# Kernel tuning notes

Hardware: AMD Instinct MI355X
Metric: run time of the kernel (lower is better)

The kernel has to match this reference:

```python
import jax, jax.numpy as jnp
import numpy as np

B, T, D, H, L = 64, 512, 512, 512, 2


def setup_inputs() -> dict:
    key = jax.random.key(0)
    ks = jax.random.split(key, 9)
    std = 1.0 / np.sqrt(H)
    u = lambda k, shape: jax.random.uniform(k, shape, jnp.float32, -std, std)
    return {
        "x": jax.random.normal(ks[0], (B, T, D), jnp.float32),
        "Wx0": u(ks[1], (4 * H, D)), "bx0": u(ks[2], (4 * H,)),
        "Wh0": u(ks[3], (4 * H, H)), "bh0": u(ks[4], (4 * H,)),
        "Wx1": u(ks[5], (4 * H, H)), "bx1": u(ks[6], (4 * H,)),
        "Wh1": u(ks[7], (4 * H, H)), "bh1": u(ks[8], (4 * H,)),
    }


def _lstm_layer(x_seq, Wx, bx, Wh, bh):
    # x_seq: [T, B, D_in] -> hidden sequence [T, B, H]
    h0 = jnp.zeros((x_seq.shape[1], Wh.shape[1]), x_seq.dtype)
    c0 = jnp.zeros_like(h0)
    # precompute input projections for all steps (one big GEMM)
    xg = jnp.einsum('tbd,gd->tbg', x_seq, Wx) + bx + bh  # [T, B, 4H]

    def step(carry, xg_t):
        h, c = carry
        gates = xg_t + h @ Wh.T
        f, i, g, o = jnp.split(gates, 4, axis=1)
        f = jax.nn.sigmoid(f)
        i = jax.nn.sigmoid(i)
        g = jnp.tanh(g)
        o = jax.nn.sigmoid(o)
        c = f * c + i * g
        h = o * jnp.tanh(c)
        return (h, c), h

    (_, _), hs = jax.lax.scan(step, (h0, c0), xg)
    return hs


def reference(x, Wx0, bx0, Wh0, bh0, Wx1, bx1, Wh1, bh1):
    xs = jnp.transpose(x, (1, 0, 2))  # [T, B, D]
    h1 = _lstm_layer(xs, Wx0, bx0, Wh0, bh0)   # [T, B, H]
    h2 = _lstm_layer(h1, Wx1, bx1, Wh1, bh1)   # [T, B, H]
    return h2[-1]  # last hidden state of top layer: [B, H]
```

## Files before the change

kernel.cpp:

```cpp
#include <hip/hip_runtime.h>
#include <hip/hip_bf16.h>
#include <stdint.h>

#define T_STEPS 512
#define BATCH   64
#define HID     512
#define DIN     512
#define G4      2048
#define HBLK_T  32768
#define SENT8   0xFFFFFFFFFFFFFFFFull

typedef __attribute__((ext_vector_type(8))) short bf16x8;
typedef __attribute__((ext_vector_type(4))) float f32x4;
typedef __attribute__((ext_vector_type(4))) unsigned short us4;

static __device__ __forceinline__ unsigned short f2bf(float f) {
  union { float f; unsigned u; } v; v.f = f;
  unsigned r = v.u + 0x7FFFu + ((v.u >> 16) & 1u);
  return (unsigned short)(r >> 16);
}
static __device__ __forceinline__ float bf2f(unsigned short s) {
  union { unsigned u; float f; } v; v.u = ((unsigned)s) << 16;
  return v.f;
}
static __device__ __forceinline__ float sigf(float x) { return 1.f / (1.f + __expf(-x)); }
static __device__ __forceinline__ float tanh_fast(float x) {
  x = fminf(15.f, fmaxf(-15.f, x));
  float e = __expf(2.f * x);
  return (e - 1.f) / (e + 1.f);
}

__global__ void cvt_f32_bf16(const float* __restrict__ src, unsigned short* __restrict__ dst, long n) {
  long i = (long)blockIdx.x * blockDim.x + threadIdx.x;
  long st = (long)gridDim.x * blockDim.x;
  for (; i < n; i += st) dst[i] = f2bf(src[i]);
}

__global__ void bias_sum(const float* __restrict__ a, const float* __restrict__ b,
                         float* __restrict__ o, int n) {
  int i = blockIdx.x * blockDim.x + threadIdx.x;
  if (i < n) o[i] = a[i] + b[i];
}

__global__ __launch_bounds__(256) void proj_kernel(
    const float* __restrict__ x,
    const unsigned short* __restrict__ Wb,
    const float* __restrict__ bias,
    unsigned short* __restrict__ xg) {
  __shared__ unsigned short xt[64 * 512];
  const int t   = blockIdx.x;
  const int tid = threadIdx.x;

  for (int i = 0; i < 16; ++i) {
    const int c    = i * 256 + tid;
    const int b    = c >> 6;
    const int col8 = c & 63;
    const float* src = x + ((long)b * T_STEPS + t) * DIN + col8 * 8;
    f32x4 v0 = *(const f32x4*)(src);
    f32x4 v1 = *(const f32x4*)(src + 4);
    union { unsigned short s[8]; bf16x8 v; } u;
    #pragma unroll
    for (int e = 0; e < 4; ++e) { u.s[e] = f2bf(v0[e]); u.s[4 + e] = f2bf(v1[e]); }
    const int byteoff = b * 1024 + ((col8 * 16) ^ ((b & 7) << 4));
    *(bf16x8*)((char*)xt + byteoff) = u.v;
  }
  __syncthreads();

  const int wv   = tid >> 6;
  const int lane = tid & 63;
  const int n16  = lane & 15;
  const int q    = lane >> 4;
  const int kof  = q * 8;

  for (int gt = 0; gt < 32; ++gt) {
    const int g0 = wv * 512 + gt * 16;
    const unsigned short* ap = Wb + (long)(g0 + n16) * DIN + kof;
    f32x4 acc[4];
    #pragma unroll
    for (int nb = 0; nb < 4; ++nb) acc[nb] = (f32x4){0.f, 0.f, 0.f, 0.f};
    #pragma unroll
    for (int kk = 0; kk < 16; ++kk) {
      bf16x8 a = *(const bf16x8*)(ap + kk * 32);
      const int colb = (kof + kk * 32) * 2;
      #pragma unroll
      for (int nb = 0; nb < 4; ++nb) {
        const int row = nb * 16 + n16;
        bf16x8 bv = *(const bf16x8*)((const char*)xt + row * 1024 + (colb ^ ((row & 7) << 4)));
        acc[nb] = __builtin_amdgcn_mfma_f32_16x16x32_bf16(a, bv, acc[nb], 0, 0, 0);
      }
    }
    const int m0 = q * 4;
    #pragma unroll
    for (int r = 0; r < 4; ++r) {
      const int g = g0 + m0 + r;
      const float bv = bias[g];
      long base = ((long)t * G4 + g) * BATCH + n16;
      xg[base +  0] = f2bf(acc[0][r] + bv);
      xg[base + 16] = f2bf(acc[1][r] + bv);
      xg[base + 32] = f2bf(acc[2][r] + bv);
      xg[base + 48] = f2bf(acc[3][r] + bv);
    }
  }
}

__global__ __launch_bounds__(128) void fused_rec(
    const unsigned short* __restrict__ Wh0b,
    const unsigned short* __restrict__ xg0,
    const unsigned short* __restrict__ Wx1b,
    const unsigned short* __restrict__ Wh1b,
    const float* __restrict__ bs1,
    unsigned short* __restrict__ hseq1,
    unsigned short* __restrict__ hseq2,
    float* __restrict__ out,
    int T) {
  __shared__ unsigned short whl0[32 * 512];
  __shared__ unsigned short whl1[32 * 1024];
  __shared__ __align__(16) unsigned short hsc[2][128];

  const int bid  = blockIdx.x;
  const int gq   = bid & 3;
  const int j    = bid >> 2;
  const int wv   = threadIdx.x >> 6;
  const int lane = threadIdx.x & 63;
  const int hidbase = j * 8;
  const int n16  = lane & 15;
  const int q    = lane >> 4;
  const int kof  = q * 8;
  const int bloc = q * 4;
  const int rr0 = n16, rr1 = 16 + n16;
  const int grow0 = (rr0 >> 3) * HID + hidbase + (rr0 & 7);
  const int grow1 = (rr1 >> 3) * HID + hidbase + (rr1 & 7);
  const int rdbase = gq * 128 + n16 * 8;
  const int myblk  = (j * 4 + gq) * 128;

  if (wv == 0) {
    #pragma unroll 4
    for (int r = 0; r < 32; ++r) {
      const long grow = (long)(r >> 3) * HID + hidbase + (r & 7);
      bf16x8 v = *(const bf16x8*)(Wh0b + grow * HID + lane * 8);
      const int off = r * 1024 + ((lane * 16) ^ ((r & 7) << 4));
      *(bf16x8*)((char*)whl0 + off) = v;
    }
  } else {
    #pragma unroll 2
    for (int r = 0; r < 32; ++r) {
      const long grow = (long)(r >> 3) * HID + hidbase + (r & 7);
      bf16x8 va = *(const bf16x8*)(Wx1b + grow * HID + lane * 8);
      bf16x8 vb = *(const bf16x8*)(Wh1b + grow * HID + lane * 8);
      const int rb = r * 2048;
      *(bf16x8*)((char*)whl1 + rb + ((lane * 16) ^ ((r & 7) << 4))) = va;
      *(bf16x8*)((char*)whl1 + rb + ((1024 + lane * 16) ^ ((r & 7) << 4))) = vb;
    }
  }
  __syncthreads();

  if (wv == 0) {
    float c[4] = {0.f, 0.f, 0.f, 0.f};
    for (int t = 0; t < T; ++t) {
      us4 xv0 = *(const us4*)(xg0 + ((long)t * G4 + grow0) * BATCH + gq * 16 + bloc);
      us4 xv1 = *(const us4*)(xg0 + ((long)t * G4 + grow1) * BATCH + gq * 16 + bloc);

      f32x4 acc0 = {0.f,0.f,0.f,0.f}, acc1 = {0.f,0.f,0.f,0.f};
      if (t > 0) {
        const unsigned long long* hp = (const unsigned long long*)
            (hseq1 + (long)(t - 1) * HBLK_T + rdbase);
        unsigned long long lo[16], hi[16];
        int bad;
        do {
          bad = 0;
          #pragma unroll
          for (int kk = 0; kk < 16; ++kk) {
            const int boff = (kk * 4 + q) * 128;
            lo[kk] = __hip_atomic_load(hp + boff,     __ATOMIC_RELAXED, __HIP_MEMORY_SCOPE_AGENT);
            hi[kk] = __hip_atomic_load(hp + boff + 1, __ATOMIC_RELAXED, __HIP_MEMORY_SCOPE_AGENT);
          }
          #pragma unroll
          for (int kk = 0; kk < 16; ++kk)
            bad |= (lo[kk] == SENT8) | (hi[kk] == SENT8);
        } while (__any(bad));
        #pragma unroll
        for (int kk = 0; kk < 16; ++kk) {
          union { unsigned long long qq[2]; bf16x8 v; } u;
          u.qq[0] = lo[kk]; u.qq[1] = hi[kk];
          const int colb = (kof + kk * 32) * 2;
          bf16x8 b0 = *(const bf16x8*)((const char*)whl0 + rr0 * 1024 + (colb ^ ((rr0 & 7) << 4)));
          bf16x8 b1 = *(const bf16x8*)((const char*)whl0 + rr1 * 1024 + (colb ^ ((rr1 & 7) << 4)));
          acc0 = __builtin_amdgcn_mfma_f32_16x16x32_bf16(u.v, b0, acc0, 0, 0, 0);
          acc1 = __builtin_amdgcn_mfma_f32_16x16x32_bf16(u.v, b1, acc1, 0, 0, 0);
        }
      }
      #pragma unroll
      for (int r = 0; r < 4; ++r) { acc0[r] += bf2f(xv0[r]); acc1[r] += bf2f(xv1[r]); }

      f32x4 o0, o1;
      #pragma unroll
      for (int r = 0; r < 4; ++r) {
        o0[r] = __shfl_xor(acc0[r], 8, 64);
        o1[r] = __shfl_xor(acc1[r], 8, 64);
      }
      if (n16 < 8) {
        #pragma unroll
        for (int r = 0; r < 4; ++r) {
          const float fg = sigf(acc0[r]);
          const float ig = sigf(o0[r]);
          const float gg = tanh_fast(acc1[r]);
          const float og = sigf(o1[r]);
          const float cn = fg * c[r] + ig * gg;
          c[r] = cn;
          const float h = og * tanh_fast(cn);
          *(unsigned short*)((char*)hsc[0] + (bloc + r) * 16 + n16 * 2) = f2bf(h);
        }
      }
      asm volatile("s_waitcnt lgkmcnt(0)" ::: "memory");
      if (lane < 32) {
        unsigned long long v8 = *(const unsigned long long*)((const char*)hsc[0] + lane * 8);
        unsigned long long* dst = (unsigned long long*)
            (hseq1 + (long)t * HBLK_T + myblk) + lane;
        __hip_atomic_store(dst, v8, __ATOMIC_RELAXED, __HIP_MEMORY_SCOPE_AGENT);
      }
    }
  } else {
    float c[4] = {0.f, 0.f, 0.f, 0.f};
    const float b0v = bs1[grow0], b1v = bs1[grow1];
    for (int t = 0; t < T; ++t) {
      f32x4 acc0 = {0.f,0.f,0.f,0.f}, acc1 = {0.f,0.f,0.f,0.f};
      {
        const unsigned long long* hp = (const unsigned long long*)
            (hseq1 + (long)t * HBLK_T + rdbase);
        unsigned long long lo[16], hi[16];
        int bad;
        do {
          bad = 0;
          #pragma unroll
          for (int kk = 0; kk < 16; ++kk) {
            const int boff = (kk * 4 + q) * 128;
            lo[kk] = __hip_atomic_load(hp + boff,     __ATOMIC_RELAXED, __HIP_MEMORY_SCOPE_AGENT);
            hi[kk] = __hip_atomic_load(hp + boff + 1, __ATOMIC_RELAXED, __HIP_MEMORY_SCOPE_AGENT);
          }
          #pragma unroll
          for (int kk = 0; kk < 16; ++kk)
            bad |= (lo[kk] == SENT8) | (hi[kk] == SENT8);
        } while (__any(bad));
        #pragma unroll
        for (int kk = 0; kk < 16; ++kk) {
          union { unsigned long long qq[2]; bf16x8 v; } u;
          u.qq[0] = lo[kk]; u.qq[1] = hi[kk];
          const int colb = (kof + kk * 32) * 2;
          bf16x8 b0 = *(const bf16x8*)((const char*)whl1 + rr0 * 2048 + (colb ^ ((rr0 & 7) << 4)));
          bf16x8 b1 = *(const bf16x8*)((const char*)whl1 + rr1 * 2048 + (colb ^ ((rr1 & 7) << 4)));
          acc0 = __builtin_amdgcn_mfma_f32_16x16x32_bf16(u.v, b0, acc0, 0, 0, 0);
          acc1 = __builtin_amdgcn_mfma_f32_16x16x32_bf16(u.v, b1, acc1, 0, 0, 0);
        }
      }
      if (t > 0) {
        const unsigned long long* hp = (const unsigned long long*)
            (hseq2 + (long)(t - 1) * HBLK_T + rdbase);
        unsigned long long lo[16], hi[16];
        int bad;
        do {
          bad = 0;
          #pragma unroll
          for (int kk = 0; kk < 16; ++kk) {
            const int boff = (kk * 4 + q) * 128;
            lo[kk] = __hip_atomic_load(hp + boff,     __ATOMIC_RELAXED, __HIP_MEMORY_SCOPE_AGENT);
            hi[kk] = __hip_atomic_load(hp + boff + 1, __ATOMIC_RELAXED, __HIP_MEMORY_SCOPE_AGENT);
          }
          #pragma unroll
          for (int kk = 0; kk < 16; ++kk)
            bad |= (lo[kk] == SENT8) | (hi[kk] == SENT8);
        } while (__any(bad));
        #pragma unroll
        for (int kk = 0; kk < 16; ++kk) {
          union { unsigned long long qq[2]; bf16x8 v; } u;
          u.qq[0] = lo[kk]; u.qq[1] = hi[kk];
          const int colb = 1024 + (kof + kk * 32) * 2;
          bf16x8 b0 = *(const bf16x8*)((const char*)whl1 + rr0 * 2048 + (colb ^ ((rr0 & 7) << 4)));
          bf16x8 b1 = *(const bf16x8*)((const char*)whl1 + rr1 * 2048 + (colb ^ ((rr1 & 7) << 4)));
          acc0 = __builtin_amdgcn_mfma_f32_16x16x32_bf16(u.v, b0, acc0, 0, 0, 0);
          acc1 = __builtin_amdgcn_mfma_f32_16x16x32_bf16(u.v, b1, acc1, 0, 0, 0);
        }
      }
      #pragma unroll
      for (int r = 0; r < 4; ++r) { acc0[r] += b0v; acc1[r] += b1v; }

      f32x4 o0, o1;
      #pragma unroll
      for (int r = 0; r < 4; ++r) {
        o0[r] = __shfl_xor(acc0[r], 8, 64);
        o1[r] = __shfl_xor(acc1[r], 8, 64);
      }
      if (n16 < 8) {
        const int hid = hidbase + n16;
        #pragma unroll
        for (int r = 0; r < 4; ++r) {
          const float fg = sigf(acc0[r]);
          const float ig = sigf(o0[r]);
          const float gg = tanh_fast(acc1[r]);
          const float og = sigf(o1[r]);
          const float cn = fg * c[r] + ig * gg;
          c[r] = cn;
          const float h = og * tanh_fast(cn);
          *(unsigned short*)((char*)hsc[1] + (bloc + r) * 16 + n16 * 2) = f2bf(h);
          if (t == T - 1) out[(long)(gq * 16 + bloc + r) * HID + hid] = h;
        }
      }
      asm volatile("s_waitcnt lgkmcnt(0)" ::: "memory");
      if (lane < 32) {
        unsigned long long v8 = *(const unsigned long long*)((const char*)hsc[1] + lane * 8);
        unsigned long long* dst = (unsigned long long*)
            (hseq2 + (long)t * HBLK_T + myblk) + lane;
        __hip_atomic_store(dst, v8, __ATOMIC_RELAXED, __HIP_MEMORY_SCOPE_AGENT);
      }
    }
  }
}

extern "C" void kernel_launch(void* const* d_in, const int* in_sizes, int n_in,
                              void* d_out, int out_size, void* d_ws, size_t ws_size,
                              hipStream_t stream) {
  const float* x   = (const float*)d_in[0];
  const float* Wx0 = (const float*)d_in[1];
  const float* bx0 = (const float*)d_in[2];
  const float* Wh0 = (const float*)d_in[3];
  const float* bh0 = (const float*)d_in[4];
  const float* Wx1 = (const float*)d_in[5];
  const float* bx1 = (const float*)d_in[6];
  const float* Wh1 = (const float*)d_in[7];
  const float* bh1 = (const float*)d_in[8];

  char* ws = (char*)d_ws;
  size_t off = 0;
  auto alloc = [&](size_t bytes) -> char* {
    char* p = ws + off; off += (bytes + 255) & ~(size_t)255; return p;
  };
  unsigned short* xg    = (unsigned short*)alloc((size_t)T_STEPS * G4 * BATCH * 2);
  unsigned short* hseq1 = (unsigned short*)alloc((size_t)T_STEPS * HBLK_T * 2);
  unsigned short* hseq2 = (unsigned short*)alloc((size_t)T_STEPS * HBLK_T * 2);
  unsigned short* Wx0b  = (unsigned short*)alloc((size_t)G4 * DIN * 2);
  unsigned short* Wh0b  = (unsigned short*)alloc((size_t)G4 * HID * 2);
  unsigned short* Wx1b  = (unsigned short*)alloc((size_t)G4 * HID * 2);
  unsigned short* Wh1b  = (unsigned short*)alloc((size_t)G4 * HID * 2);
  float* bs0 = (float*)alloc((size_t)G4 * 4);
  float* bs1 = (float*)alloc((size_t)G4 * 4);

  hipMemsetAsync(hseq1, 0xFF, (size_t)T_STEPS * HBLK_T * 2, stream);
  hipMemsetAsync(hseq2, 0xFF, (size_t)T_STEPS * HBLK_T * 2, stream);

  cvt_f32_bf16<<<1024, 256, 0, stream>>>(Wx0, Wx0b, (long)G4 * DIN);
  cvt_f32_bf16<<<1024, 256, 0, stream>>>(Wh0, Wh0b, (long)G4 * HID);
  cvt_f32_bf16<<<1024, 256, 0, stream>>>(Wx1, Wx1b, (long)G4 * HID);
  cvt_f32_bf16<<<1024, 256, 0, stream>>>(Wh1, Wh1b, (long)G4 * HID);
  bias_sum<<<8, 256, 0, stream>>>(bx0, bh0, bs0, G4);
  bias_sum<<<8, 256, 0, stream>>>(bx1, bh1, bs1, G4);

  proj_kernel<<<T_STEPS, 256, 0, stream>>>(x, Wx0b, bs0, xg);
  fused_rec<<<256, 128, 0, stream>>>(Wh0b, xg, Wx1b, Wh1b, bs1,
                                     hseq1, hseq2, (float*)d_out, T_STEPS);
}
```

Before: 2.043 ms.

## Fuse layer-0 input projection into recurrent kernel via producer wave and LDS ring

The separate projection GEMM and the weight and bias conversion kernels are removed. A third wave in each recurrent block now computes the layer-0 input projection for its own gate rows step by step and hands the results to the layer-0 wave through a 16-slot shared-memory ring, synchronised with workgroup-scope flags. Weights are converted from fp32 inside the kernel, and the h-sequence loads are issued before waiting on the ring. This removes the large xg round trip through global memory and several launches, but adds an extra wave per block and intra-block spin waits.

New measurement: 2.278 ms. 11.5% more time.

```diff
diff --git a/kernel.cpp b/kernel.cpp
--- a/kernel.cpp
+++ b/kernel.cpp
@@ -8,11 +8,13 @@
 #define DIN     512
 #define G4      2048
 #define HBLK_T  32768
+#define RING    16
 #define SENT8   0xFFFFFFFFFFFFFFFFull
 
 typedef __attribute__((ext_vector_type(8))) short bf16x8;
 typedef __attribute__((ext_vector_type(4))) float f32x4;
 typedef __attribute__((ext_vector_type(4))) unsigned short us4;
+typedef unsigned long long ull;
 
 static __device__ __forceinline__ unsigned short f2bf(float f) {
   union { float f; unsigned u; } v; v.f = f;
@@ -30,92 +32,38 @@
   return (e - 1.f) / (e + 1.f);
 }
 
-__global__ void cvt_f32_bf16(const float* __restrict__ src, unsigned short* __restrict__ dst, long n) {
-  long i = (long)blockIdx.x * blockDim.x + threadIdx.x;
-  long st = (long)gridDim.x * blockDim.x;
-  for (; i < n; i += st) dst[i] = f2bf(src[i]);
-}
-
-__global__ void bias_sum(const float* __restrict__ a, const float* __restrict__ b,
-                         float* __restrict__ o, int n) {
-  int i = blockIdx.x * blockDim.x + threadIdx.x;
-  if (i < n) o[i] = a[i] + b[i];
-}
-
-__global__ __launch_bounds__(256) void proj_kernel(
-    const float* __restrict__ x,
-    const unsigned short* __restrict__ Wb,
-    const float* __restrict__ bias,
-    unsigned short* __restrict__ xg) {
-  __shared__ unsigned short xt[64 * 512];
-  const int t   = blockIdx.x;
-  const int tid = threadIdx.x;
-
-  for (int i = 0; i < 16; ++i) {
-    const int c    = i * 256 + tid;
-    const int b    = c >> 6;
-    const int col8 = c & 63;
-    const float* src = x + ((long)b * T_STEPS + t) * DIN + col8 * 8;
-    f32x4 v0 = *(const f32x4*)(src);
-    f32x4 v1 = *(const f32x4*)(src + 4);
-    union { unsigned short s[8]; bf16x8 v; } u;
-    #pragma unroll
-    for (int e = 0; e < 4; ++e) { u.s[e] = f2bf(v0[e]); u.s[4 + e] = f2bf(v1[e]); }
-    const int byteoff = b * 1024 + ((col8 * 16) ^ ((b & 7) << 4));
-    *(bf16x8*)((char*)xt + byteoff) = u.v;
-  }
-  __syncthreads();
-
-  const int wv   = tid >> 6;
-  const int lane = tid & 63;
-  const int n16  = lane & 15;
-  const int q    = lane >> 4;
-  const int kof  = q * 8;
-
-  for (int gt = 0; gt < 32; ++gt) {
-    const int g0 = wv * 512 + gt * 16;
-    const unsigned short* ap = Wb + (long)(g0 + n16) * DIN + kof;
-    f32x4 acc[4];
-    #pragma unroll
-    for (int nb = 0; nb < 4; ++nb) acc[nb] = (f32x4){0.f, 0.f, 0.f, 0.f};
-    #pragma unroll
-    for (int kk = 0; kk < 16; ++kk) {
-      bf16x8 a = *(const bf16x8*)(ap + kk * 32);
-      const int colb = (kof + kk * 32) * 2;
-      #pragma unroll
-      for (int nb = 0; nb < 4; ++nb) {
-        const int row = nb * 16 + n16;
-        bf16x8 bv = *(const bf16x8*)((const char*)xt + row * 1024 + (colb ^ ((row & 7) << 4)));
-        acc[nb] = __builtin_amdgcn_mfma_f32_16x16x32_bf16(a, bv, acc[nb], 0, 0, 0);
-      }
-    }
-    const int m0 = q * 4;
-    #pragma unroll
-    for (int r = 0; r < 4; ++r) {
-      const int g = g0 + m0 + r;
-      const float bv = bias[g];
-      long base = ((long)t * G4 + g) * BATCH + n16;
-      xg[base +  0] = f2bf(acc[0][r] + bv);
-      xg[base + 16] = f2bf(acc[1][r] + bv);
-      xg[base + 32] = f2bf(acc[2][r] + bv);
-      xg[base + 48] = f2bf(acc[3][r] + bv);
-    }
-  }
-}
-
-__global__ __launch_bounds__(128) void fused_rec(
-    const unsigned short* __restrict__ Wh0b,
-    const unsigned short* __restrict__ xg0,
-    const unsigned short* __restrict__ Wx1b,
-    const unsigned short* __restrict__ Wh1b,
-    const float* __restrict__ bs1,
+__global__ __launch_bounds__(256) void xb_cvt(const float* __restrict__ x,
+                                              unsigned short* __restrict__ xb) {
+  const long c  = (long)blockIdx.x * blockDim.x + threadIdx.x;
+  const int b   = (int)(c >> 15);
+  const int rem = (int)(c & 32767);
+  const int t   = rem >> 6;
+  const int k8  = rem & 63;
+  const float* src = x + ((long)b * T_STEPS + t) * DIN + k8 * 8;
+  f32x4 v0 = *(const f32x4*)src;
+  f32x4 v1 = *(const f32x4*)(src + 4);
+  union { unsigned short s[8]; bf16x8 v; } u;
+  #pragma unroll
+  for (int e = 0; e < 4; ++e) { u.s[e] = f2bf(v0[e]); u.s[4 + e] = f2bf(v1[e]); }
+  *(bf16x8*)(xb + ((long)t * BATCH + b) * DIN + k8 * 8) = u.v;
+}
+
+__global__ __launch_bounds__(192, 1) void fused_rec(
+    const float* __restrict__ Wh0, const float* __restrict__ Wx0,
+    const float* __restrict__ Wh1, const float* __restrict__ Wx1,
+    const float* __restrict__ bx0, const float* __restrict__ bh0,
+    const float* __restrict__ bx1, const float* __restrict__ bh1,
+    const unsigned short* __restrict__ xb,
     unsigned short* __restrict__ hseq1,
     unsigned short* __restrict__ hseq2,
     float* __restrict__ out,
     int T) {
+  __shared__ unsigned short wx0l[32 * 512];
   __shared__ unsigned short whl0[32 * 512];
   __shared__ unsigned short whl1[32 * 1024];
+  __shared__ __align__(16) unsigned short ring[RING][512];
   __shared__ __align__(16) unsigned short hsc[2][128];
+  __shared__ int p_done, l0_done;
 
   const int bid  = blockIdx.x;
   const int gq   = bid & 3;
@@ -133,55 +81,76 @@
   const int rdbase = gq * 128 + n16 * 8;
   const int myblk  = (j * 4 + gq) * 128;
 
+  if (threadIdx.x == 0) { p_done = 0; l0_done = 0; }
+
+  auto cv8 = [](const float* s) -> bf16x8 {
+    f32x4 a = *(const f32x4*)s, b = *(const f32x4*)(s + 4);
+    union { unsigned short u[8]; bf16x8 v; } w;
+    #pragma unroll
+    for (int e = 0; e < 4; ++e) { w.u[e] = f2bf(a[e]); w.u[4 + e] = f2bf(b[e]); }
+    return w.v;
+  };
   if (wv == 0) {
-    #pragma unroll 4
     for (int r = 0; r < 32; ++r) {
       const long grow = (long)(r >> 3) * HID + hidbase + (r & 7);
-      bf16x8 v = *(const bf16x8*)(Wh0b + grow * HID + lane * 8);
-      const int off = r * 1024 + ((lane * 16) ^ ((r & 7) << 4));
-      *(bf16x8*)((char*)whl0 + off) = v;
-    }
-  } else {
-    #pragma unroll 2
+      bf16x8 v = cv8(Wh0 + grow * HID + lane * 8);
+      *(bf16x8*)((char*)whl0 + r * 1024 + ((lane * 16) ^ ((r & 7) << 4))) = v;
+    }
+  } else if (wv == 1) {
     for (int r = 0; r < 32; ++r) {
       const long grow = (long)(r >> 3) * HID + hidbase + (r & 7);
-      bf16x8 va = *(const bf16x8*)(Wx1b + grow * HID + lane * 8);
-      bf16x8 vb = *(const bf16x8*)(Wh1b + grow * HID + lane * 8);
+      bf16x8 va = cv8(Wx1 + grow * HID + lane * 8);
+      bf16x8 vb = cv8(Wh1 + grow * HID + lane * 8);
       const int rb = r * 2048;
       *(bf16x8*)((char*)whl1 + rb + ((lane * 16) ^ ((r & 7) << 4))) = va;
       *(bf16x8*)((char*)whl1 + rb + ((1024 + lane * 16) ^ ((r & 7) << 4))) = vb;
     }
+  } else {
+    for (int r = 0; r < 32; ++r) {
+      const long grow = (long)(r >> 3) * HID + hidbase + (r & 7);
+      bf16x8 v = cv8(Wx0 + grow * HID + lane * 8);
+      *(bf16x8*)((char*)wx0l + r * 1024 + ((lane * 16) ^ ((r & 7) << 4))) = v;
+    }
   }
   __syncthreads();
 
   if (wv == 0) {
-    float c[4] = {0.f, 0.f, 0.f, 0.f};
+    float c4[4] = {0.f, 0.f, 0.f, 0.f};
     for (int t = 0; t < T; ++t) {
-      us4 xv0 = *(const us4*)(xg0 + ((long)t * G4 + grow0) * BATCH + gq * 16 + bloc);
-      us4 xv1 = *(const us4*)(xg0 + ((long)t * G4 + grow1) * BATCH + gq * 16 + bloc);
+      ull lo[16], hi[16];
+      const ull* hp = (const ull*)(hseq1 + (long)(t - 1) * HBLK_T + rdbase);
+      if (t > 0) {
+        #pragma unroll
+        for (int kk = 0; kk < 16; ++kk) {
+          const int boff = (kk * 4 + q) * 128;
+          lo[kk] = __hip_atomic_load(hp + boff,     __ATOMIC_RELAXED, __HIP_MEMORY_SCOPE_AGENT);
+          hi[kk] = __hip_atomic_load(hp + boff + 1, __ATOMIC_RELAXED, __HIP_MEMORY_SCOPE_AGENT);
+        }
+      }
+      while (__hip_atomic_load(&p_done, __ATOMIC_ACQUIRE, __HIP_MEMORY_SCOPE_WORKGROUP) < t + 1) {}
+      const int s = t & (RING - 1);
+      us4 xv0 = *(const us4*)&ring[s][n16 * 16 + q * 4];
+      us4 xv1 = *(const us4*)&ring[s][(16 + n16) * 16 + q * 4];
+      if (lane == 0)
+        __hip_atomic_store(&l0_done, t + 1, __ATOMIC_RELEASE, __HIP_MEMORY_SCOPE_WORKGROUP);
 
       f32x4 acc0 = {0.f,0.f,0.f,0.f}, acc1 = {0.f,0.f,0.f,0.f};
       if (t > 0) {
-        const unsigned long long* hp = (const unsigned long long*)
-            (hseq1 + (long)(t - 1) * HBLK_T + rdbase);
-        unsigned long long lo[16], hi[16];
-        int bad;
-        do {
-          bad = 0;
+        for (;;) {
+          int bad = 0;
+          #pragma unroll
+          for (int kk = 0; kk < 16; ++kk) bad |= (lo[kk] == SENT8) | (hi[kk] == SENT8);
+          if (!__any(bad)) break;
           #pragma unroll
           for (int kk = 0; kk < 16; ++kk) {
             const int boff = (kk * 4 + q) * 128;
             lo[kk] = __hip_atomic_load(hp + boff,     __ATOMIC_RELAXED, __HIP_MEMORY_SCOPE_AGENT);
             hi[kk] = __hip_atomic_load(hp + boff + 1, __ATOMIC_RELAXED, __HIP_MEMORY_SCOPE_AGENT);
           }
-          #pragma unroll
-          for (int kk = 0; kk < 16; ++kk)
-            bad |= (lo[kk] == SENT8) | (hi[kk] == SENT8);
-        } while (__any(bad));
-        #pragma unroll
-        for (int kk = 0; kk < 16; ++kk) {
-          union { unsigned long long qq[2]; bf16x8 v; } u;
-          u.qq[0] = lo[kk]; u.qq[1] = hi[kk];
+        }
+        #pragma unroll
+        for (int kk = 0; kk < 16; ++kk) {
+          union { ull qq[2]; bf16x8 v; } u; u.qq[0] = lo[kk]; u.qq[1] = hi[kk];
           const int colb = (kof + kk * 32) * 2;
           bf16x8 b0 = *(const bf16x8*)((const char*)whl0 + rr0 * 1024 + (colb ^ ((rr0 & 7) << 4)));
           bf16x8 b1 = *(const bf16x8*)((const char*)whl0 + rr1 * 1024 + (colb ^ ((rr1 & 7) << 4)));
@@ -205,74 +174,79 @@
           const float ig = sigf(o0[r]);
           const float gg = tanh_fast(acc1[r]);
           const float og = sigf(o1[r]);
-          const float cn = fg * c[r] + ig * gg;
-          c[r] = cn;
+          const float cn = fg * c4[r] + ig * gg;
+          c4[r] = cn;
           const float h = og * tanh_fast(cn);
           *(unsigned short*)((char*)hsc[0] + (bloc + r) * 16 + n16 * 2) = f2bf(h);
         }
       }
       asm volatile("s_waitcnt lgkmcnt(0)" ::: "memory");
       if (lane < 32) {
-        unsigned long long v8 = *(const unsigned long long*)((const char*)hsc[0] + lane * 8);
-        unsigned long long* dst = (unsigned long long*)
-            (hseq1 + (long)t * HBLK_T + myblk) + lane;
+        ull v8 = *(const ull*)((const char*)hsc[0] + lane * 8);
+        ull* dst = (ull*)(hseq1 + (long)t * HBLK_T + myblk) + lane;
         __hip_atomic_store(dst, v8, __ATOMIC_RELAXED, __HIP_MEMORY_SCOPE_AGENT);
       }
     }
-  } else {
-    float c[4] = {0.f, 0.f, 0.f, 0.f};
-    const float b0v = bs1[grow0], b1v = bs1[grow1];
+  } else if (wv == 1) {
+    float c4[4] = {0.f, 0.f, 0.f, 0.f};
+    const float b0v = bx1[grow0] + bh1[grow0];
+    const float b1v = bx1[grow1] + bh1[grow1];
     for (int t = 0; t < T; ++t) {
+      ull la[16], ha[16], lb[16], hb[16];
+      const ull* pa = (const ull*)(hseq1 + (long)t * HBLK_T + rdbase);
+      const ull* pb = (const ull*)(hseq2 + (long)(t - 1) * HBLK_T + rdbase);
+      #pragma unroll
+      for (int kk = 0; kk < 16; ++kk) {
+        const int boff = (kk * 4 + q) * 128;
+        la[kk] = __hip_atomic_load(pa + boff,     __ATOMIC_RELAXED, __HIP_MEMORY_SCOPE_AGENT);
+        ha[kk] = __hip_atomic_load(pa + boff + 1, __ATOMIC_RELAXED, __HIP_MEMORY_SCOPE_AGENT);
+      }
+      if (t > 0) {
+        #pragma unroll
+        for (int kk = 0; kk < 16; ++kk) {
+          const int boff = (kk * 4 + q) * 128;
+          lb[kk] = __hip_atomic_load(pb + boff,     __ATOMIC_RELAXED, __HIP_MEMORY_SCOPE_AGENT);
+          hb[kk] = __hip_atomic_load(pb + boff + 1, __ATOMIC_RELAXED, __HIP_MEMORY_SCOPE_AGENT);
+        }
+      }
+      for (;;) {
+        int bad = 0;
+        #pragma unroll
+        for (int kk = 0; kk < 16; ++kk) bad |= (la[kk] == SENT8) | (ha[kk] == SENT8);
+        if (!__any(bad)) break;
+        #pragma unroll
+        for (int kk = 0; kk < 16; ++kk) {
+          const int boff = (kk * 4 + q) * 128;
+          la[kk] = __hip_atomic_load(pa + boff,     __ATOMIC_RELAXED, __HIP_MEMORY_SCOPE_AGENT);
+          ha[kk] = __hip_atomic_load(pa + boff + 1, __ATOMIC_RELAXED, __HIP_MEMORY_SCOPE_AGENT);
+        }
+      }
       f32x4 acc0 = {0.f,0.f,0.f,0.f}, acc1 = {0.f,0.f,0.f,0.f};
-      {
-        const unsigned long long* hp = (const unsigned long long*)
-            (hseq1 + (long)t * HBLK_T + rdbase);
-        unsigned long long lo[16], hi[16];
-        int bad;
-        do {
-          bad = 0;
+      #pragma unroll
+      for (int kk = 0; kk < 16; ++kk) {
+        union { ull qq[2]; bf16x8 v; } u; u.qq[0] = la[kk]; u.qq[1] = ha[kk];
+        const int colb = (kof + kk * 32) * 2;
+        bf16x8 b0 = *(const bf16x8*)((const char*)whl1 + rr0 * 2048 + (colb ^ ((rr0 & 7) << 4)));
+        bf16x8 b1 = *(const bf16x8*)((const char*)whl1 + rr1 * 2048 + (colb ^ ((rr1 & 7) << 4)));
+        acc0 = __builtin_amdgcn_mfma_f32_16x16x32_bf16(u.v, b0, acc0, 0, 0, 0);
+        acc1 = __builtin_amdgcn_mfma_f32_16x16x32_bf16(u.v, b1, acc1, 0, 0, 0);
+      }
+      if (t > 0) {
+        for (;;) {
+          int bad = 0;
+          #pragma unroll
+          for (int kk = 0; kk < 16; ++kk) bad |= (lb[kk] == SENT8) | (hb[kk] == SENT8);
+          if (!__any(bad)) break;
           #pragma unroll
           for (int kk = 0; kk < 16; ++kk) {
             const int boff = (kk * 4 + q) * 128;
-            lo[kk] = __hip_atomic_load(hp + boff,     __ATOMIC_RELAXED, __HIP_MEMORY_SCOPE_AGENT);
-            hi[kk] = __hip_atomic_load(hp + boff + 1, __ATOMIC_RELAXED, __HIP_MEMORY_SCOPE_AGENT);
+            lb[kk] = __hip_atomic_load(pb + boff,     __ATOMIC_RELAXED, __HIP_MEMORY_SCOPE_AGENT);
+            hb[kk] = __hip_atomic_load(pb + boff + 1, __ATOMIC_RELAXED, __HIP_MEMORY_SCOPE_AGENT);
           }
-          #pragma unroll
-          for (int kk = 0; kk < 16; ++kk)
-            bad |= (lo[kk] == SENT8) | (hi[kk] == SENT8);
-        } while (__any(bad));
-        #pragma unroll
-        for (int kk = 0; kk < 16; ++kk) {
-          union { unsigned long long qq[2]; bf16x8 v; } u;
-          u.qq[0] = lo[kk]; u.qq[1] = hi[kk];
-          const int colb = (kof + kk * 32) * 2;
-          bf16x8 b0 = *(const bf16x8*)((const char*)whl1 + rr0 * 2048 + (colb ^ ((rr0 & 7) << 4)));
-          bf16x8 b1 = *(const bf16x8*)((const char*)whl1 + rr1 * 2048 + (colb ^ ((rr1 & 7) << 4)));
-          acc0 = __builtin_amdgcn_mfma_f32_16x16x32_bf16(u.v, b0, acc0, 0, 0, 0);
-          acc1 = __builtin_amdgcn_mfma_f32_16x16x32_bf16(u.v, b1, acc1, 0, 0, 0);
-        }
-      }
-      if (t > 0) {
-        const unsigned long long* hp = (const unsigned long long*)
-            (hseq2 + (long)(t - 1) * HBLK_T + rdbase);
-        unsigned long long lo[16], hi[16];
-        int bad;
-        do {
-          bad = 0;
-          #pragma unroll
-          for (int kk = 0; kk < 16; ++kk) {
-            const int boff = (kk * 4 + q) * 128;
-            lo[kk] = __hip_atomic_load(hp + boff,     __ATOMIC_RELAXED, __HIP_MEMORY_SCOPE_AGENT);
-            hi[kk] = __hip_atomic_load(hp + boff + 1, __ATOMIC_RELAXED, __HIP_MEMORY_SCOPE_AGENT);
-          }
-          #pragma unroll
-          for (int kk = 0; kk < 16; ++kk)
-            bad |= (lo[kk] == SENT8) | (hi[kk] == SENT8);
-        } while (__any(bad));
-        #pragma unroll
-        for (int kk = 0; kk < 16; ++kk) {
-          union { unsigned long long qq[2]; bf16x8 v; } u;
-          u.qq[0] = lo[kk]; u.qq[1] = hi[kk];
+        }
+        #pragma unroll
+        for (int kk = 0; kk < 16; ++kk) {
+          union { ull qq[2]; bf16x8 v; } u; u.qq[0] = lb[kk]; u.qq[1] = hb[kk];
           const int colb = 1024 + (kof + kk * 32) * 2;
           bf16x8 b0 = *(const bf16x8*)((const char*)whl1 + rr0 * 2048 + (colb ^ ((rr0 & 7) << 4)));
           bf16x8 b1 = *(const bf16x8*)((const char*)whl1 + rr1 * 2048 + (colb ^ ((rr1 & 7) << 4)));
@@ -297,8 +271,8 @@
           const float ig = sigf(o0[r]);
           const float gg = tanh_fast(acc1[r]);
           const float og = sigf(o1[r]);
-          const float cn = fg * c[r] + ig * gg;
-          c[r] = cn;
+          const float cn = fg * c4[r] + ig * gg;
+          c4[r] = cn;
           const float h = og * tanh_fast(cn);
           *(unsigned short*)((char*)hsc[1] + (bloc + r) * 16 + n16 * 2) = f2bf(h);
           if (t == T - 1) out[(long)(gq * 16 + bloc + r) * HID + hid] = h;
@@ -306,11 +280,39 @@
       }
       asm volatile("s_waitcnt lgkmcnt(0)" ::: "memory");
       if (lane < 32) {
-        unsigned long long v8 = *(const unsigned long long*)((const char*)hsc[1] + lane * 8);
-        unsigned long long* dst = (unsigned long long*)
-            (hseq2 + (long)t * HBLK_T + myblk) + lane;
+        ull v8 = *(const ull*)((const char*)hsc[1] + lane * 8);
+        ull* dst = (ull*)(hseq2 + (long)t * HBLK_T + myblk) + lane;
         __hip_atomic_store(dst, v8, __ATOMIC_RELAXED, __HIP_MEMORY_SCOPE_AGENT);
       }
+    }
+  } else {
+    const float bsP0 = bx0[grow0] + bh0[grow0];
+    const float bsP1 = bx0[grow1] + bh0[grow1];
+    for (int t = 0; t < T; ++t) {
+      while (t - __hip_atomic_load(&l0_done, __ATOMIC_RELAXED, __HIP_MEMORY_SCOPE_WORKGROUP) >= RING)
+        __builtin_amdgcn_s_sleep(1);
+      const unsigned short* xp = xb + ((long)t * BATCH + gq * 16 + n16) * DIN + kof;
+      f32x4 a0 = {0.f,0.f,0.f,0.f}, a1 = {0.f,0.f,0.f,0.f};
+      #pragma unroll
+      for (int kk = 0; kk < 16; ++kk) {
+        bf16x8 av = *(const bf16x8*)(xp + kk * 32);
+        const int colb = (kof + kk * 32) * 2;
+        bf16x8 b0 = *(const bf16x8*)((const char*)wx0l + rr0 * 1024 + (colb ^ ((rr0 & 7) << 4)));
+        bf16x8 b1 = *(const bf16x8*)((const char*)wx0l + rr1 * 1024 + (colb ^ ((rr1 & 7) << 4)));
+        a0 = __builtin_amdgcn_mfma_f32_16x16x32_bf16(av, b0, a0, 0, 0, 0);
+        a1 = __builtin_amdgcn_mfma_f32_16x16x32_bf16(av, b1, a1, 0, 0, 0);
+      }
+      us4 w0, w1;
+      #pragma unroll
+      for (int r = 0; r < 4; ++r) {
+        w0[r] = f2bf(a0[r] + bsP0);
+        w1[r] = f2bf(a1[r] + bsP1);
+      }
+      const int s = t & (RING - 1);
+      *(us4*)&ring[s][n16 * 16 + q * 4] = w0;
+      *(us4*)&ring[s][(16 + n16) * 16 + q * 4] = w1;
+      if (lane == 0)
+        __hip_atomic_store(&p_done, t + 1, __ATOMIC_RELEASE, __HIP_MEMORY_SCOPE_WORKGROUP);
     }
   }
 }
@@ -333,27 +335,16 @@
   auto alloc = [&](size_t bytes) -> char* {
     char* p = ws + off; off += (bytes + 255) & ~(size_t)255; return p;
   };
-  unsigned short* xg    = (unsigned short*)alloc((size_t)T_STEPS * G4 * BATCH * 2);
+  unsigned short* xb    = (unsigned short*)alloc((size_t)T_STEPS * BATCH * DIN * 2);
   unsigned short* hseq1 = (unsigned short*)alloc((size_t)T_STEPS * HBLK_T * 2);
   unsigned short* hseq2 = (unsigned short*)alloc((size_t)T_STEPS * HBLK_T * 2);
-  unsigned short* Wx0b  = (unsigned short*)alloc((size_t)G4 * DIN * 2);
-  unsigned short* Wh0b  = (unsigned short*)alloc((size_t)G4 * HID * 2);
-  unsigned short* Wx1b  = (unsigned short*)alloc((size_t)G4 * HID * 2);
-  unsigned short* Wh1b  = (unsigned short*)alloc((size_t)G4 * HID * 2);
-  float* bs0 = (float*)alloc((size_t)G4 * 4);
-  float* bs1 = (float*)alloc((size_t)G4 * 4);
 
   hipMemsetAsync(hseq1, 0xFF, (size_t)T_STEPS * HBLK_T * 2, stream);
   hipMemsetAsync(hseq2, 0xFF, (size_t)T_STEPS * HBLK_T * 2, stream);
 
-  cvt_f32_bf16<<<1024, 256, 0, stream>>>(Wx0, Wx0b, (long)G4 * DIN);
-  cvt_f32_bf16<<<1024, 256, 0, stream>>>(Wh0, Wh0b, (long)G4 * HID);
-  cvt_f32_bf16<<<1024, 256, 0, stream>>>(Wx1, Wx1b, (long)G4 * HID);
-  cvt_f32_bf16<<<1024, 256, 0, stream>>>(Wh1, Wh1b, (long)G4 * HID);
-  bias_sum<<<8, 256, 0, stream>>>(bx0, bh0, bs0, G4);
-  bias_sum<<<8, 256, 0, stream>>>(bx1, bh1, bs1, G4);
-
-  proj_kernel<<<T_STEPS, 256, 0, stream>>>(x, Wx0b, bs0, xg);
-  fused_rec<<<256, 128, 0, stream>>>(Wh0b, xg, Wx1b, Wh1b, bs1,
-                                     hseq1, hseq2, (float*)d_out, T_STEPS);
-}
+  xb_cvt<<<8192, 256, 0, stream>>>(x, xb);
+
+  fused_rec<<<256, 192, 0, stream>>>(Wh0, Wx0, Wh1, Wx1,
+                                     bx0, bh0, bx1, bh1,
+                                     xb, hseq1, hseq2, (float*)d_out, T_STEPS);
+}
```
